# Optimization experiments

Hardware: AMD Instinct MI355X
Metric: run time of the kernel (lower is better)

## Reference

```python
import jax, jax.numpy as jnp
import numpy as np

ALPHA, BETA, INIT_P = 100.0, 1000.0, 2.0
K_NEIGHBORS = 24


def index_points(pts, idx):
    # pts: [B,N,C], idx: [B,...] int -> [B,...,C]
    B = pts.shape[0]
    b = jnp.arange(B).reshape((B,) + (1,) * (idx.ndim - 1))
    return pts[b, idx]


def fps(xyz, m):
    # furthest point sampling, deterministic start at index 0. xyz: [B,N,3]
    B, N, _ = xyz.shape
    def step(carry, _):
        dist, far = carry
        centroid = xyz[jnp.arange(B), far]              # [B,3]
        d = jnp.sum((xyz - centroid[:, None, :]) ** 2, -1)
        dist = jnp.minimum(dist, d)
        nxt = jnp.argmax(dist, -1).astype(jnp.int32)
        return (dist, nxt), far
    init = (jnp.full((B, N), 1e10, xyz.dtype), jnp.zeros((B,), jnp.int32))
    _, idx = jax.lax.scan(step, init, None, length=m)
    return idx.T                                        # [B,m]


def knn_indices(k, xyz, centers):
    # squared distances [B,G,N], k smallest
    d = (jnp.sum(centers ** 2, -1)[..., None]
         - 2.0 * jnp.einsum('bgc,bnc->bgn', centers, xyz)
         + jnp.sum(xyz ** 2, -1)[:, None, :])
    _, idx = jax.lax.top_k(-d, k)
    return idx                                          # [B,G,K]


def normalize(x, ref):
    # torch: mean = ref.unsqueeze(-2); std over ALL elements of (x-mean), ddof=1
    d = x - ref[..., None, :]
    std = jnp.std(d, ddof=1)
    return d / (std + 1e-5)


def fourier_map(t, Bmat):
    # t: [B,7,G,K]; Bmat: [7, C//2] (already includes scale) -> [B,C,G,K]
    x = jnp.transpose(t, (0, 2, 3, 1))                  # [B,G,K,7]
    proj = 2.0 * jnp.pi * (x @ Bmat)                    # [B,G,K,C/2]
    f = jnp.concatenate([jnp.sin(proj), jnp.cos(proj)], -1)
    f = jnp.sign(f) * jnp.abs(f) ** 5
    return jnp.transpose(f, (0, 3, 1, 2))


def tr_embed(my_dim, t):
    # t: [B,3,G,K] -> [B,my_dim,G,K]
    B, C, G, K = t.shape
    F = my_dim // (2 * C)
    dim_embed = ALPHA ** (jnp.arange(F, dtype=t.dtype) / F)
    div = BETA * t[..., None] / dim_embed               # [B,3,G,K,F]
    pe = jnp.stack([jnp.sin(div), jnp.cos(div)], -1).reshape(B, C, G, K, 2 * F)
    pe = jnp.transpose(pe, (0, 1, 4, 2, 3)).reshape(B, my_dim, G, K)
    return pe


def lga(lc_xyz, lc_x, knn_xyz, knn_x, Bmat):
    B, G, K, C = knn_x.shape
    knn_x = normalize(knn_x, lc_x)
    knn_xyz = normalize(knn_xyz, lc_xyz)
    lc_rep = jnp.transpose(jnp.broadcast_to(lc_xyz[:, :, None, :], (B, G, K, 3)), (0, 3, 1, 2))
    knn_xyz_t = jnp.transpose(knn_xyz, (0, 3, 1, 2))    # [B,3,G,K]
    knn_x_t = jnp.transpose(knn_x, (0, 3, 1, 2))        # [B,C,G,K]
    cross = jnp.cross(knn_xyz_t, lc_rep, axis=1)
    dot = jnp.sum(knn_xyz_t * lc_rep, 1, keepdims=True)
    emb_in = jnp.concatenate([knn_xyz_t, cross, dot], 1)  # [B,7,G,K]
    emb = fourier_map(emb_in, Bmat)                       # [B,C,G,K]
    knn_x_w = jnp.concatenate([knn_x_t, emb], 1)          # [B,2C,G,K]
    pe = tr_embed(2 * C, knn_xyz_t) + tr_embed(2 * C, lc_rep)
    return (knn_x_w + pe) * pe


def k_anp(x):
    # x: [B,2C,G,K], data-dependent p-norm attention over K
    std = jnp.std(x, axis=-1, ddof=1, keepdims=True)
    p = jax.lax.stop_gradient(INIT_P + jnp.log1p(std.mean()))  # torch uses .item()
    norm = jnp.sum(jnp.abs(x) ** p, -1, keepdims=True) ** (1.0 / p)
    lc = norm / (norm + 1e-8)
    e = jnp.exp(lc)
    return (x * e).mean(-1) / e.mean(-1)                # [B,2C,G]


def bn_gelu(x, gamma, beta):
    # BatchNorm1d in training mode (batch stats, biased var) + exact GELU
    mean = x.mean((0, 2), keepdims=True)
    var = ((x - mean) ** 2).mean((0, 2), keepdims=True)
    y = (x - mean) / jnp.sqrt(var + 1e-5) * gamma[None, :, None] + beta[None, :, None]
    return jax.nn.gelu(y, approximate=False)


def stage(xyz, x, group_num, Bmat, gamma, beta):
    # xyz: [B,N,3]; x: [B,C,N]
    feats = jnp.transpose(x, (0, 2, 1))
    fi = fps(xyz, group_num)
    lc_xyz = index_points(xyz, fi)
    lc_x = index_points(feats, fi)
    ki = knn_indices(K_NEIGHBORS, xyz, lc_xyz)
    knn_xyz = index_points(xyz, ki)
    knn_x = index_points(feats, ki)
    w = lga(lc_xyz, lc_x, knn_xyz, knn_x, Bmat)
    pooled = k_anp(w) + w.mean(-1)                      # [B,2C,G]
    return lc_xyz, bn_gelu(pooled, gamma, beta)


def setup_inputs() -> dict:
    key = jax.random.key(0)
    k1, k2, k3, k4 = jax.random.split(key, 4)
    B, N, C0 = 4, 4096, 72
    return {
        'xyz': jax.random.uniform(k1, (B, N, 3), jnp.float32),
        'x': jax.random.normal(k2, (B, C0, N), jnp.float32),
        'fourier_B0': jax.random.normal(k3, (7, C0 // 2), jnp.float32) * 50.0,
        'fourier_B1': jax.random.normal(k4, (7, C0), jnp.float32) * 50.0,
        'bn_gamma0': jnp.ones((2 * C0,), jnp.float32),
        'bn_beta0': jnp.zeros((2 * C0,), jnp.float32),
        'bn_gamma1': jnp.ones((4 * C0,), jnp.float32),
        'bn_beta1': jnp.zeros((4 * C0,), jnp.float32),
    }


def reference(xyz, x, fourier_B0, fourier_B1, bn_gamma0, bn_beta0, bn_gamma1, bn_beta1):
    N = xyz.shape[1]
    xyz, x = stage(xyz, x, N // 2, fourier_B0, bn_gamma0, bn_beta0)   # -> [B,144,2048]
    xyz, x = stage(xyz, x, N // 4, fourier_B1, bn_gamma1, bn_beta1)   # -> [B,288,1024]
    return x
```

## Files before the change

kernel.cpp:

```cpp
#include <hip/hip_runtime.h>
#include <math.h>

#define KNB 24

typedef float v2f __attribute__((ext_vector_type(2)));

template<int CTRL>
__device__ __forceinline__ float dppmax(float v) {
    int t = __builtin_amdgcn_update_dpp(0, __float_as_int(v), CTRL, 0xf, 0xf, true);
    return fmaxf(v, __int_as_float(t));
}
template<int CTRL>
__device__ __forceinline__ unsigned dppmaxu(unsigned v) {
    unsigned t = (unsigned)__builtin_amdgcn_update_dpp(0, (int)v, CTRL, 0xf, 0xf, true);
    return v > t ? v : t;
}
template<int CTRL>
__device__ __forceinline__ double dppmax64(double v) {
    unsigned long long u = __double_as_longlong(v);
    int lo = (int)(unsigned)(u & 0xffffffffull);
    int hi = (int)(unsigned)(u >> 32);
    int tlo = __builtin_amdgcn_update_dpp(0, lo, CTRL, 0xf, 0xf, true);
    int thi = __builtin_amdgcn_update_dpp(0, hi, CTRL, 0xf, 0xf, true);
    double t = __longlong_as_double(((unsigned long long)(unsigned)thi << 32) | (unsigned)tlo);
    return __builtin_fmax(v, t);
}

template<int NPT, int NWAVE>
__global__ __launch_bounds__(64 * NWAVE, 1) void k_fps_tr(const float* __restrict__ xyz,
                                                          int* __restrict__ fi,
                                                          int N, int M,
                                                          const float* __restrict__ x0,
                                                          float* __restrict__ feats,
                                                          int C, int NT, int nT, int cT) {
#pragma clang fp contract(off)
    const int NP2 = NPT / 2;
    const int tid = threadIdx.x;
    extern __shared__ char smc[];

    if ((int)blockIdx.x >= 4) {
        int bid = blockIdx.x - 4;
        int tilesPerB = nT * cT;
        int b = bid / tilesPerB;
        int t2 = bid - b * tilesPerB;
        int cTile = t2 / nT;
        int nTile = t2 - cTile * nT;
        int tx = tid & 31, ty = tid >> 5;
        const int ROWS = 2 * NWAVE;
        float* tile = (float*)smc;
        for (int r = ty; r < 32; r += ROWS) {
            int c = cTile * 32 + r, n = nTile * 32 + tx;
            if (c < C && n < NT) tile[r * 33 + tx] = x0[((size_t)b * C + c) * NT + n];
        }
        __syncthreads();
        for (int r = ty; r < 32; r += ROWS) {
            int n = nTile * 32 + r, c = cTile * 32 + tx;
            if (c < C && n < NT) feats[((size_t)b * NT + n) * C + c] = tile[tx * 33 + r];
        }
        return;
    }

    const int b = blockIdx.x;
    const int lane = tid & 63;
    const int wid = tid >> 6;
    unsigned long long* keys = (unsigned long long*)smc;
    int* fi_lds = (int*)(smc + 2 * NWAVE * 8);
    size_t poff = ((size_t)(2 * NWAVE * 8) + (size_t)M * 4 + 15) & ~(size_t)15;
    float4* pts = (float4*)(smc + poff);

    const float* p = xyz + (size_t)b * N * 3;
    for (int i = tid; i < N; i += 64 * NWAVE)
        pts[i] = make_float4(p[i*3], p[i*3+1], p[i*3+2], 0.0f);
    __syncthreads();

    const int base = tid * NPT;
    v2f rx[NP2], ry[NP2], rz[NP2], dist[NP2];
    unsigned lowc[NPT];
#pragma unroll
    for (int j = 0; j < NP2; ++j) {
        float4 a = pts[base + 2*j];
        float4 c = pts[base + 2*j + 1];
        rx[j] = (v2f){a.x, c.x}; ry[j] = (v2f){a.y, c.y}; rz[j] = (v2f){a.z, c.z};
        dist[j] = (v2f){1e10f, 1e10f};
        lowc[2*j]   = ~(unsigned)(base + 2*j);
        lowc[2*j+1] = ~(unsigned)(base + 2*j + 1);
    }

    int far = 0;
    float4 cpt = pts[0];
    float cx = cpt.x, cy = cpt.y, cz = cpt.z;
    for (int it = 0; it < M; ++it) {
        if (tid == 0) fi_lds[it] = far;
        v2f cx2 = (v2f){cx, cx}, cy2 = (v2f){cy, cy}, cz2 = (v2f){cz, cz};
        double kA = 0.0, kB = 0.0;
#pragma unroll
        for (int j = 0; j < NP2; ++j) {
            v2f dx = rx[j] - cx2, dy = ry[j] - cy2, dz = rz[j] - cz2;
            v2f d = (dx*dx + dy*dy) + dz*dz;
            v2f dd = __builtin_elementwise_min(dist[j], d);
            dist[j] = dd;
            double k0 = __longlong_as_double(
                ((unsigned long long)__float_as_uint(dd.x) << 32) | lowc[2*j]);
            double k1 = __longlong_as_double(
                ((unsigned long long)__float_as_uint(dd.y) << 32) | lowc[2*j+1]);
            kA = __builtin_fmax(kA, k0);
            kB = __builtin_fmax(kB, k1);
        }
        double km = __builtin_fmax(kA, kB);
        km = dppmax64<0x111>(km); km = dppmax64<0x112>(km);
        km = dppmax64<0x114>(km); km = dppmax64<0x118>(km);
        km = dppmax64<0x142>(km); km = dppmax64<0x143>(km);
        if (lane == 63) keys[(it & 1) * NWAVE + wid] = __double_as_longlong(km);
        __syncthreads();
        const unsigned long long* kk = keys + (it & 1) * NWAVE;
        double g;
        if (NWAVE == 8) {
            double m0 = __builtin_fmax(__longlong_as_double(kk[0]), __longlong_as_double(kk[1]));
            double m1 = __builtin_fmax(__longlong_as_double(kk[2]), __longlong_as_double(kk[3]));
            double m2 = __builtin_fmax(__longlong_as_double(kk[4]), __longlong_as_double(kk[5]));
            double m3 = __builtin_fmax(__longlong_as_double(kk[6]), __longlong_as_double(kk[7]));
            m0 = __builtin_fmax(m0, m1);
            m2 = __builtin_fmax(m2, m3);
            g = __builtin_fmax(m0, m2);
        } else {
            g = __longlong_as_double(kk[0]);
#pragma unroll
            for (int w = 1; w < NWAVE; ++w)
                g = __builtin_fmax(g, __longlong_as_double(kk[w]));
        }
        far = (int)(~(unsigned)__double_as_longlong(g));
        float4 c = pts[far];
        cx = c.x; cy = c.y; cz = c.z;
    }
    __syncthreads();
    for (int i = tid; i < M; i += 64 * NWAVE) fi[b * M + i] = fi_lds[i];
}

template<int NPT>
__global__ __launch_bounds__(256) void k_knn_t(const float* __restrict__ xyz,
                                               const float* __restrict__ feats,
                                               const int* __restrict__ fi,
                                               float* __restrict__ lc_xyz,
                                               float* __restrict__ lc_x,
                                               int* __restrict__ ki,
                                               double* __restrict__ part,
                                               int B, int N, int G, int C, int identity) {
#pragma clang fp contract(off)
    int bg = blockIdx.x; int b = bg / G; int g = bg % G;
    int idx = identity ? g : fi[bg];
    const int tid = threadIdx.x;
    const int lane = tid & 63;
    const int wid = tid >> 6;
    __shared__ unsigned long long keys[2][4];
    __shared__ int kis[KNB];
    __shared__ float cfeat[144];
    const float* p = xyz + (size_t)b * N * 3;
    float cx = p[idx*3], cy = p[idx*3+1], cz = p[idx*3+2];
    if (tid < 3) lc_xyz[(size_t)bg * 3 + tid] = p[idx*3 + tid];
    for (int c = tid; c < C; c += 256) {
        float v = feats[((size_t)b * N + idx) * C + c];
        lc_x[(size_t)bg * C + c] = v;
        cfeat[c] = v;
    }
    float cc = (cx*cx + cy*cy) + cz*cz;
    const int base = tid * NPT;
    float dist[NPT];
#pragma unroll
    for (int j = 0; j < NPT; ++j) {
        float x0 = p[(base+j)*3], x1 = p[(base+j)*3+1], x2 = p[(base+j)*3+2];
        float xx = (x0*x0 + x1*x1) + x2*x2;
        float dt = (cx*x0 + cy*x1) + cz*x2;
        dist[j] = (cc - 2.0f*dt) + xx;
    }
    for (int kk = 0; kk < KNB; ++kk) {
        float bv = 1e30f;
#pragma unroll
        for (int j = 0; j < NPT; ++j) bv = fminf(bv, dist[j]);
        int lj = 0;
#pragma unroll
        for (int j = NPT - 1; j >= 0; --j) if (dist[j] == bv) lj = j;
        unsigned ub = ~__float_as_uint(bv);
        unsigned r = ub;
        r = dppmaxu<0x111>(r); r = dppmaxu<0x112>(r);
        r = dppmaxu<0x114>(r); r = dppmaxu<0x118>(r);
        r = dppmaxu<0x142>(r); r = dppmaxu<0x143>(r);
        unsigned uwin = (unsigned)__builtin_amdgcn_readlane((int)r, 63);
        unsigned long long mask = __ballot(ub == uwin);
        int src = __builtin_ctzll(mask);
        int gi = __builtin_amdgcn_readlane(base + lj, src);
        unsigned long long key = ((unsigned long long)uwin << 32) | (unsigned)(~gi);
        if (lane == 0) keys[kk & 1][wid] = key;
        __syncthreads();
        unsigned long long k0 = keys[kk & 1][0];
#pragma unroll
        for (int w = 1; w < 4; ++w) {
            unsigned long long kw = keys[kk & 1][w];
            if (kw > k0) k0 = kw;
        }
        int win = (int)(~(unsigned)k0);
        if (tid == 0) kis[kk] = win;
        if (win >= base && win < base + NPT) {
            int wj = win - base;
#pragma unroll
            for (int j = 0; j < NPT; ++j) if (j == wj) dist[j] = 1e30f;
        }
    }
    __syncthreads();
    if (tid < KNB) ki[(size_t)bg * KNB + tid] = kis[tid];
    double s = 0.0, s2 = 0.0, s3 = 0.0, s4 = 0.0;
    for (int i = tid; i < KNB * C; i += 256) {
        int k = i / C, c = i - k * C;
        float d = feats[((size_t)b * N + kis[k]) * C + c] - cfeat[c];
        s += (double)d; s2 += (double)d * (double)d;
    }
    if (tid < KNB * 3) {
        int k = tid / 3, c = tid - k * 3;
        float ctr = (c == 0) ? cx : ((c == 1) ? cy : cz);
        float d = p[kis[k] * 3 + c] - ctr;
        s3 += (double)d; s4 += (double)d * (double)d;
    }
    for (int off = 32; off > 0; off >>= 1) {
        s += __shfl_down(s, off); s2 += __shfl_down(s2, off);
        s3 += __shfl_down(s3, off); s4 += __shfl_down(s4, off);
    }
    __shared__ double sw[4][4];
    if ((tid & 63) == 0) {
        sw[wid][0] = s; sw[wid][1] = s2; sw[wid][2] = s3; sw[wid][3] = s4;
    }
    __syncthreads();
    if (tid == 0) {
        double t0 = 0.0, t1 = 0.0, t2 = 0.0, t3 = 0.0;
        for (int w = 0; w < 4; ++w) {
            t0 += sw[w][0]; t1 += sw[w][1]; t2 += sw[w][2]; t3 += sw[w][3];
        }
        double* q = part + (size_t)bg * 4;
        q[0] = t0; q[1] = t1; q[2] = t2; q[3] = t3;
    }
}

__global__ __launch_bounds__(1024) void k_reduce(const double* __restrict__ part,
                                                 double* __restrict__ acc, int n) {
    double s0 = 0.0, s1 = 0.0, s2 = 0.0, s3 = 0.0;
    for (int i = threadIdx.x; i < n; i += 1024) {
        const double* q = part + (size_t)i * 4;
        s0 += q[0]; s1 += q[1]; s2 += q[2]; s3 += q[3];
    }
    for (int off = 32; off > 0; off >>= 1) {
        s0 += __shfl_down(s0, off); s1 += __shfl_down(s1, off);
        s2 += __shfl_down(s2, off); s3 += __shfl_down(s3, off);
    }
    __shared__ double sw[16][4];
    int wid = threadIdx.x >> 6;
    if ((threadIdx.x & 63) == 0) {
        sw[wid][0] = s0; sw[wid][1] = s1; sw[wid][2] = s2; sw[wid][3] = s3;
    }
    __syncthreads();
    if (threadIdx.x == 0) {
        double t0 = 0.0, t1 = 0.0, t2 = 0.0, t3 = 0.0;
        for (int w = 0; w < 16; ++w) {
            t0 += sw[w][0]; t1 += sw[w][1]; t2 += sw[w][2]; t3 += sw[w][3];
        }
        acc[0] = t0; acc[1] = t1; acc[2] = t2; acc[3] = t3;
    }
}

__global__ __launch_bounds__(256) void k_feature(
    const float* __restrict__ xyz, const float* __restrict__ feats,
    const float* __restrict__ lc_xyz, const float* __restrict__ lc_x,
    const int* __restrict__ ki, const float* __restrict__ Bmat,
    const double* __restrict__ accp, float* __restrict__ pooled,
    int B, int N, int G, int C, double nx, double nz)
{
    int bg = blockIdx.x; int b = bg / G; int g = bg % G;
    int tid = threadIdx.x;
    int C2 = C >> 1;
    int Cout = 2 * C;
    int F = C / 3;
    extern __shared__ float sm[];
    float* t7    = sm;
    float* sxyzn = t7 + KNB * 7;
    int*   kidx  = (int*)(sxyzn + KNB * 3);
    float* semb  = (float*)(kidx + KNB);
    float* sfeat = semb + KNB * C;

    double a0 = accp[0], a1 = accp[1], a2 = accp[2], a3 = accp[3];
    double vx = (a1 - a0 * a0 / nx) / (nx - 1.0);
    float invx = 1.0f / (sqrtf((float)vx) + 1e-5f);
    double vz = (a3 - a2 * a2 / nz) / (nz - 1.0);
    float invz = 1.0f / (sqrtf((float)vz) + 1e-5f);

    float l0 = lc_xyz[(size_t)bg*3], l1 = lc_xyz[(size_t)bg*3+1], l2 = lc_xyz[(size_t)bg*3+2];

    if (tid < KNB) {
        int idx = ki[(size_t)bg * KNB + tid];
        kidx[tid] = idx;
        const float* q = xyz + ((size_t)b * N + idx) * 3;
        float a0f = (q[0]-l0)*invz, a1f = (q[1]-l1)*invz, a2f = (q[2]-l2)*invz;
        float c0 = a1f*l2 - a2f*l1;
        float c1 = a2f*l0 - a0f*l2;
        float c2 = a0f*l1 - a1f*l0;
        float dt = (a0f*l0 + a1f*l1) + a2f*l2;
        float* tp = t7 + tid * 7;
        tp[0]=a0f; tp[1]=a1f; tp[2]=a2f; tp[3]=c0; tp[4]=c1; tp[5]=c2; tp[6]=dt;
        sxyzn[tid*3]=a0f; sxyzn[tid*3+1]=a1f; sxyzn[tid*3+2]=a2f;
    }
    __syncthreads();
    for (int i = tid; i < KNB * C; i += blockDim.x) {
        int k = i / C, c = i - k * C;
        sfeat[i] = feats[((size_t)b * N + kidx[k]) * C + c];
    }
    const float TWO_PI = 6.2831854820251465f;
    for (int i = tid; i < KNB * C2; i += blockDim.x) {
        int k = i / C2, m2 = i % C2;
        const float* tp = t7 + k * 7;
        float s = 0.0f;
        for (int j = 0; j < 7; ++j) s += tp[j] * Bmat[j * C2 + m2];
        float pr = TWO_PI * s;
        float sn, cs;
        __sincosf(pr, &sn, &cs);
        float sn2 = sn*sn, cs2 = cs*cs;
        semb[k*C + m2]      = sn2*sn2*sn;
        semb[k*C + C2 + m2] = cs2*cs2*cs;
    }
    __syncthreads();
    for (int m = tid; m < Cout; m += blockDim.x) {
        int c3 = m / (2 * F);
        int r  = m % (2 * F);
        int f  = r >> 1;
        int trig = r & 1;
        float de = __powf(100.0f, (float)f / (float)F);
        float rde = 1000.0f / de;
        float lv = (c3 == 0) ? l0 : ((c3 == 1) ? l1 : l2);
        float a2v = lv * rde;
        float pe2 = trig ? __cosf(a2v) : __sinf(a2v);
        float lfm = (m < C) ? lc_x[(size_t)bg * C + m] : 0.0f;
        float acc = 0.0f;
        for (int k = 0; k < KNB; ++k) {
            float v;
            if (m < C) {
                v = (sfeat[k * C + m] - lfm) * invx;
            } else {
                v = semb[k * C + (m - C)];
            }
            float a1v = sxyzn[k*3 + c3] * rde;
            float pe1 = trig ? __cosf(a1v) : __sinf(a1v);
            float pe = pe1 + pe2;
            acc += (v + pe) * pe;
        }
        float mean = acc / 24.0f;
        pooled[((size_t)b * Cout + m) * G + g] = 2.0f * mean;
    }
}

__global__ __launch_bounds__(256) void k_bn(const float* __restrict__ pooled,
                                            const float* __restrict__ gamma,
                                            const float* __restrict__ beta,
                                            float* __restrict__ out,
                                            int B, int Cout, int G, int transposed) {
    int m = blockIdx.x;
    double s = 0.0, s2 = 0.0;
    for (int i = threadIdx.x; i < B * G; i += 256) {
        int b = i / G, g = i % G;
        float v = pooled[((size_t)b * Cout + m) * G + g];
        s += (double)v; s2 += (double)v * (double)v;
    }
    for (int off = 32; off > 0; off >>= 1) { s += __shfl_down(s, off); s2 += __shfl_down(s2, off); }
    __shared__ double sw[4], sw2[4];
    __shared__ float smv[2];
    int wid = threadIdx.x >> 6;
    if ((threadIdx.x & 63) == 0) { sw[wid] = s; sw2[wid] = s2; }
    __syncthreads();
    if (threadIdx.x == 0) {
        double ts = sw[0] + sw[1] + sw[2] + sw[3];
        double ts2 = sw2[0] + sw2[1] + sw2[2] + sw2[3];
        double n = (double)(B * G);
        double mean = ts / n;
        double var = ts2 / n - mean * mean;
        smv[0] = (float)mean; smv[1] = (float)var;
    }
    __syncthreads();
    float mean = smv[0], var = smv[1];
    float ga = gamma[m], be = beta[m];
    for (int i = threadIdx.x; i < B * G; i += 256) {
        int b = i / G, g = i % G;
        float v = pooled[((size_t)b * Cout + m) * G + g];
        float y = (v - mean) / sqrtf(var + 1e-5f) * ga + be;
        float ge = 0.5f * y * (1.0f + erff(y / 1.4142135381698608f));
        if (transposed) out[((size_t)b * G + g) * Cout + m] = ge;
        else            out[((size_t)b * Cout + m) * G + g] = ge;
    }
}

extern "C" void kernel_launch(void* const* d_in, const int* in_sizes, int n_in,
                              void* d_out, int out_size, void* d_ws, size_t ws_size,
                              hipStream_t stream) {
    const int B = 4, N1 = 4096, C0 = 72, G1 = 2048, Co1 = 144;
    const int N2 = 2048, C1 = 144, G2 = 1024, Co2 = 288;

    const float* xyz = (const float*)d_in[0];
    const float* x0  = (const float*)d_in[1];
    const float* B0  = (const float*)d_in[2];
    const float* B1  = (const float*)d_in[3];
    const float* g0  = (const float*)d_in[4];
    const float* be0 = (const float*)d_in[5];
    const float* g1  = (const float*)d_in[6];
    const float* be1 = (const float*)d_in[7];
    float* out = (float*)d_out;

    char* wp = (char*)d_ws;
    size_t off = 0;
    auto A = [&](size_t bytes) -> void* {
        void* p = wp + off;
        off += (bytes + 255) & ~(size_t)255;
        return p;
    };
    float* feats1  = (float*)A((size_t)B*N1*C0*4);
    int*   fi1     = (int*)  A((size_t)B*G1*4);
    float* lcx1    = (float*)A((size_t)B*G1*3*4);
    float* lcf1    = (float*)A((size_t)B*G1*C0*4);
    int*   ki1     = (int*)  A((size_t)B*G1*KNB*4);
    double* acc    = (double*)A(8*8);
    double* part   = (double*)A((size_t)B*G1*4*8);
    float* pooled1 = (float*)A((size_t)B*Co1*G1*4);
    float* feats2  = (float*)A((size_t)B*N2*C1*4);
    float* lcx2    = (float*)A((size_t)B*G2*3*4);
    float* lcf2    = lcf1;
    int*   ki2     = ki1;
    float* pooled2 = feats1;

    {
        const int nT = N1 / 32, cT = (C0 + 31) / 32;
        const int NW = 8;
        size_t poff = ((size_t)(2*NW*8) + (size_t)G1*4 + 15) & ~(size_t)15;
        size_t shm = poff + (size_t)N1*16;
        k_fps_tr<8, NW><<<B + B*nT*cT, 64*NW, shm, stream>>>(xyz, fi1, N1, G1,
                                                             x0, feats1, C0, N1, nT, cT);
    }
    k_knn_t<16><<<B*G1, 256, 0, stream>>>(xyz, feats1, fi1, lcx1, lcf1, ki1, part,
                                          B, N1, G1, C0, 0);
    k_reduce<<<1, 1024, 0, stream>>>(part, acc, B*G1);
    {
        size_t shf = (size_t)(KNB*7 + KNB*3 + KNB + 2*KNB*C0) * 4;
        k_feature<<<B*G1, 256, shf, stream>>>(xyz, feats1, lcx1, lcf1, ki1, B0, acc, pooled1,
                                              B, N1, G1, C0,
                                              (double)B*G1*KNB*C0, (double)B*G1*KNB*3);
    }
    k_bn<<<Co1, 256, 0, stream>>>(pooled1, g0, be0, feats2, B, Co1, G1, 1);

    k_knn_t<8><<<B*G2, 256, 0, stream>>>(lcx1, feats2, (const int*)nullptr,
                                         lcx2, lcf2, ki2, part, B, N2, G2, C1, 1);
    k_reduce<<<1, 1024, 0, stream>>>(part, acc + 4, B*G2);
    {
        size_t shf = (size_t)(KNB*7 + KNB*3 + KNB + 2*KNB*C1) * 4;
        k_feature<<<B*G2, 256, shf, stream>>>(lcx1, feats2, lcx2, lcf2, ki2, B1, acc + 4, pooled2,
                                              B, N2, G2, C1,
                                              (double)B*G2*KNB*C1, (double)B*G2*KNB*3);
    }
    k_bn<<<Co2, 256, 0, stream>>>(pooled2, g1, be1, out, B, Co2, G2, 0);
}
```

Measured before the change: 1.577 ms.

## Replace per-iteration FPS block barrier with tagged LDS spin-wait reduction

Each wave's argmax key in the furthest-point-sampling loop now carries the iteration number in its low 20 bits, with the point index packed into 12 bits above it. Waves write their key to a double-buffered LDS slot and spin on volatile reads until every slot shows the current tag, instead of meeting at __syncthreads. The aim is to remove the per-iteration workgroup barrier from this long serial loop. In exchange, the index only fits if N is at most 4096, and the spinning adds extra LDS traffic.

```diff
diff --git a/kernel.cpp b/kernel.cpp
--- a/kernel.cpp
+++ b/kernel.cpp
@@ -69,6 +69,7 @@
     float4* pts = (float4*)(smc + poff);
 
     const float* p = xyz + (size_t)b * N * 3;
+    if (tid < 2 * NWAVE) keys[tid] = ~0ull;
     for (int i = tid; i < N; i += 64 * NWAVE)
         pts[i] = make_float4(p[i*3], p[i*3+1], p[i*3+2], 0.0f);
     __syncthreads();
@@ -82,8 +83,8 @@
         float4 c = pts[base + 2*j + 1];
         rx[j] = (v2f){a.x, c.x}; ry[j] = (v2f){a.y, c.y}; rz[j] = (v2f){a.z, c.z};
         dist[j] = (v2f){1e10f, 1e10f};
-        lowc[2*j]   = ~(unsigned)(base + 2*j);
-        lowc[2*j+1] = ~(unsigned)(base + 2*j + 1);
+        lowc[2*j]   = (~(unsigned)(base + 2*j)     & 0xFFFu) << 20;
+        lowc[2*j+1] = (~(unsigned)(base + 2*j + 1) & 0xFFFu) << 20;
     }
 
     int far = 0;
@@ -110,25 +111,41 @@
         km = dppmax64<0x111>(km); km = dppmax64<0x112>(km);
         km = dppmax64<0x114>(km); km = dppmax64<0x118>(km);
         km = dppmax64<0x142>(km); km = dppmax64<0x143>(km);
-        if (lane == 63) keys[(it & 1) * NWAVE + wid] = __double_as_longlong(km);
-        __syncthreads();
-        const unsigned long long* kk = keys + (it & 1) * NWAVE;
+        const unsigned tag = (unsigned)it & 0xFFFFFu;
+        if (lane == 63) {
+            unsigned long long kw = __double_as_longlong(km) | (unsigned long long)tag;
+            *((volatile unsigned long long*)&keys[(it & 1) * NWAVE + wid]) = kw;
+        }
+        volatile unsigned long long* kk =
+            (volatile unsigned long long*)(keys + (it & 1) * NWAVE);
+        unsigned long long kv[NWAVE];
+        bool ok;
+        do {
+            ok = true;
+#pragma unroll
+            for (int w = 0; w < NWAVE; ++w) {
+                kv[w] = kk[w];
+                ok &= (((unsigned)kv[w] & 0xFFFFFu) == tag);
+            }
+        } while (!ok);
         double g;
         if (NWAVE == 8) {
-            double m0 = __builtin_fmax(__longlong_as_double(kk[0]), __longlong_as_double(kk[1]));
-            double m1 = __builtin_fmax(__longlong_as_double(kk[2]), __longlong_as_double(kk[3]));
-            double m2 = __builtin_fmax(__longlong_as_double(kk[4]), __longlong_as_double(kk[5]));
-            double m3 = __builtin_fmax(__longlong_as_double(kk[6]), __longlong_as_double(kk[7]));
-            m0 = __builtin_fmax(m0, m1);
-            m2 = __builtin_fmax(m2, m3);
-            g = __builtin_fmax(m0, m2);
+            double m0 = __builtin_fmax(__longlong_as_double((long long)kv[0]),
+                                       __longlong_as_double((long long)kv[1]));
+            double m1 = __builtin_fmax(__longlong_as_double((long long)kv[2]),
+                                       __longlong_as_double((long long)kv[3]));
+            double m2 = __builtin_fmax(__longlong_as_double((long long)kv[4]),
+                                       __longlong_as_double((long long)kv[5]));
+            double m3 = __builtin_fmax(__longlong_as_double((long long)kv[6]),
+                                       __longlong_as_double((long long)kv[7]));
+            g = __builtin_fmax(__builtin_fmax(m0, m1), __builtin_fmax(m2, m3));
         } else {
-            g = __longlong_as_double(kk[0]);
+            g = __longlong_as_double((long long)kv[0]);
 #pragma unroll
             for (int w = 1; w < NWAVE; ++w)
-                g = __builtin_fmax(g, __longlong_as_double(kk[w]));
-        }
-        far = (int)(~(unsigned)__double_as_longlong(g));
+                g = __builtin_fmax(g, __longlong_as_double((long long)kv[w]));
+        }
+        far = (int)(0xFFFu ^ ((unsigned)(__double_as_longlong(g) >> 20) & 0xFFFu));
         float4 c = pts[far];
         cx = c.x; cy = c.y; cz = c.z;
     }
```

Measured after the change: 2.240 ms. +42.0%, slower.
